# Kernel tuning notes

Hardware: AMD Instinct MI355X
Metric: run time of the kernel (lower is better)

Reference implementation:

```python
import jax, jax.numpy as jnp
import numpy as np

D = 768  # hidden dim hard-coded in the module


def setup_inputs() -> dict:
    key = jax.random.key(0)
    k1, k2, k3, k4, k5 = jax.random.split(key, 5)
    N, M = 512, 512
    return {
        "text_output": jax.random.normal(k1, (N, D), dtype=jnp.float32),
        "visual_output": jax.random.normal(k2, (M, D), dtype=jnp.float32),
        "W1": jax.random.normal(k3, (D, D), dtype=jnp.float32),
        "W2": jax.random.normal(k4, (D, D), dtype=jnp.float32),
        "W3": jax.random.normal(k5, (D, D), dtype=jnp.float32),
    }


def reference(text_output, visual_output, W1, W2, W3):
    # C[n,m] = tanh( (text @ W1) . visual[m] )
    C = jnp.tanh((text_output @ W1) @ visual_output.T)            # (N, M)
    W2_text = text_output @ W2                                    # (N, D)
    W3_visual = visual_output @ W3.T                              # (M, D)
    # M[n,m,:] = tanh(W2_text[n] + W3_visual[m] * C[n,m])
    Mt = jnp.tanh(W2_text[:, None, :] + W3_visual[None, :, :] * C[..., None])  # (N, M, D)
    # score[n,m] = text[n] . M[n,m]  (replaces the per-row Python loop)
    score = jnp.einsum("nd,nmd->nm", text_output, Mt)             # (N, M)
    return score
```

## Files before the change

kernel.cpp:

```cpp
#include <hip/hip_runtime.h>

#define DD   768
#define NN   512
#define MM   512

#define PRE_K 2.88539008177792681472f

typedef _Float16 h8 __attribute__((ext_vector_type(8)));
typedef __attribute__((ext_vector_type(4))) float f32x4;

__device__ __forceinline__ float fexp(float x) { return __builtin_amdgcn_exp2f(x); }
__device__ __forceinline__ float frcp(float x) { return __builtin_amdgcn_rcpf(x); }
__device__ __forceinline__ float fast_tanh(float x) {
  return 1.0f - 2.0f * frcp(fexp(PRE_K * x) + 1.0f);
}

__device__ __forceinline__ void splitf(float x, ushort& h, ushort& l) {
  const _Float16 hh = (_Float16)x;
  const _Float16 ll = (_Float16)(x - (float)hh);
  h = __builtin_bit_cast(unsigned short, hh);
  l = __builtin_bit_cast(unsigned short, ll);
}

__global__ __launch_bounds__(256) void prep_kernel(
    const float* __restrict__ text, const float* __restrict__ visual,
    const float* __restrict__ W1, const float* __restrict__ W2,
    const float* __restrict__ W3,
    ushort* __restrict__ th, ushort* __restrict__ tl,
    ushort* __restrict__ vh, ushort* __restrict__ vl,
    ushort* __restrict__ w3h, ushort* __restrict__ w3l,
    ushort* __restrict__ w1th, ushort* __restrict__ w1tl,
    ushort* __restrict__ w2th, ushort* __restrict__ w2tl,
    float* __restrict__ out)
{
  __shared__ float Lt[32][33];
  const int b = blockIdx.x;
  const int t = threadIdx.x;

  if (b < 1344) {
    const float* src; ushort *dh, *dl; size_t off;
    if (b < 384)      { src = text;   dh = th;  dl = tl;  off = (size_t)b * 1024; }
    else if (b < 768) { src = visual; dh = vh;  dl = vl;  off = (size_t)(b - 384) * 1024; }
    else              { src = W3;     dh = w3h; dl = w3l; off = (size_t)(b - 768) * 1024; }
    const size_t i = off + (size_t)t * 4;
    const float4 v = *(const float4*)&src[i];
    ushort4 h, l;
    splitf(v.x, h.x, l.x); splitf(v.y, h.y, l.y);
    splitf(v.z, h.z, l.z); splitf(v.w, h.w, l.w);
    *(ushort4*)&dh[i] = h;
    *(ushort4*)&dl[i] = l;
  } else if (b < 2496) {
    const int tt = b - 1344;
    const bool second = tt >= 576;
    const int tile = second ? tt - 576 : tt;
    const float* W = second ? W2 : W1;
    ushort* oh = second ? w2th : w1th;
    ushort* ol = second ? w2tl : w1tl;
    const int k0 = (tile / 24) * 32, j0 = (tile % 24) * 32;
    {
      const int k = t >> 3, j4 = (t & 7) * 4;
      const float4 v = *(const float4*)&W[(size_t)(k0 + k) * DD + j0 + j4];
      Lt[j4 + 0][k] = v.x; Lt[j4 + 1][k] = v.y;
      Lt[j4 + 2][k] = v.z; Lt[j4 + 3][k] = v.w;
    }
    __syncthreads();
    {
      const int j = t >> 3, k4 = (t & 7) * 4;
      ushort4 h, l;
      splitf(Lt[j][k4 + 0], h.x, l.x); splitf(Lt[j][k4 + 1], h.y, l.y);
      splitf(Lt[j][k4 + 2], h.z, l.z); splitf(Lt[j][k4 + 3], h.w, l.w);
      *(ushort4*)&oh[(size_t)(j0 + j) * DD + k0 + k4] = h;
      *(ushort4*)&ol[(size_t)(j0 + j) * DD + k0 + k4] = l;
    }
  } else {
    float* red = (float*)Lt;
    const int u = b - 2496;
    const int n0 = u * 2;
    const int half = t >> 7;
    const int lt = t & 127;

    const float* tr = text + (size_t)(n0 + half) * DD;
    float s = 0.f;
    #pragma unroll
    for (int i = 0; i < DD / 128; ++i) s += tr[lt + i * 128];
    red[t] = s;
    __syncthreads();
    #pragma unroll
    for (int st = 64; st > 0; st >>= 1) {
      if (lt < st) red[t] += red[t + st];
      __syncthreads();
    }
    const float Tn = red[half << 7];
    float4 o; o.x = Tn; o.y = Tn; o.z = Tn; o.w = Tn;
    *(float4*)&out[(size_t)(n0 + half) * MM + lt * 4] = o;
  }
}

#define BK   32
#define LROW 40

template <bool ALO>
__device__ __forceinline__ void gemm_core(
    const ushort* __restrict__ Ahg, const ushort* __restrict__ Alg,
    const ushort* __restrict__ Bhg, const ushort* __restrict__ Blg,
    int i0, int j0, int k0, int nsteps, f32x4* acc)
{
  __shared__ ushort As[2][2][64 * LROW];
  __shared__ ushort Bs[2][2][64 * LROW];

  const int tid  = threadIdx.x;
  const int row  = tid >> 2;
  const int ks8  = (tid & 3) * 8;
  const size_t ga = (size_t)(i0 + row) * DD + k0 + ks8;
  const size_t gb = (size_t)(j0 + row) * DD + k0 + ks8;
  const int ldsw = row * LROW + ks8;

  const int lane = tid & 63, wave = tid >> 6;
  const int r15 = lane & 15, quad = lane >> 4;
  const int fa = (wave * 16 + r15) * LROW + quad * 8;
  const int fb = r15 * LROW + quad * 8;

  h8 pah = *(const h8*)(Ahg + ga);
  h8 pal; if (ALO) pal = *(const h8*)(Alg + ga);
  h8 pbh = *(const h8*)(Bhg + gb);
  h8 pbl = *(const h8*)(Blg + gb);

  int p = 0;
  *(h8*)&As[0][0][ldsw] = pah;
  if (ALO) *(h8*)&As[0][1][ldsw] = pal;
  *(h8*)&Bs[0][0][ldsw] = pbh; *(h8*)&Bs[0][1][ldsw] = pbl;
  __syncthreads();

  for (int s = 0; s < nsteps; ++s) {
    const bool more = (s + 1 < nsteps);
    if (more) {
      pah = *(const h8*)(Ahg + ga + (s + 1) * BK);
      if (ALO) pal = *(const h8*)(Alg + ga + (s + 1) * BK);
      pbh = *(const h8*)(Bhg + gb + (s + 1) * BK);
      pbl = *(const h8*)(Blg + gb + (s + 1) * BK);
    }
    const h8 a_h = *(const h8*)&As[p][0][fa];
    h8 a_l; if (ALO) a_l = *(const h8*)&As[p][1][fa];
    h8 b_h[4], b_l[4];
    #pragma unroll
    for (int c = 0; c < 4; ++c) {
      b_h[c] = *(const h8*)&Bs[p][0][fb + c * 16 * LROW];
      b_l[c] = *(const h8*)&Bs[p][1][fb + c * 16 * LROW];
    }
    #pragma unroll
    for (int c = 0; c < 4; ++c)
      acc[c] = __builtin_amdgcn_mfma_f32_16x16x32_f16(a_h, b_h[c], acc[c], 0, 0, 0);
    #pragma unroll
    for (int c = 0; c < 4; ++c)
      acc[c] = __builtin_amdgcn_mfma_f32_16x16x32_f16(a_h, b_l[c], acc[c], 0, 0, 0);
    if (ALO) {
      #pragma unroll
      for (int c = 0; c < 4; ++c)
        acc[c] = __builtin_amdgcn_mfma_f32_16x16x32_f16(a_l, b_h[c], acc[c], 0, 0, 0);
    }
    if (more) {
      const int q = p ^ 1;
      *(h8*)&As[q][0][ldsw] = pah;
      if (ALO) *(h8*)&As[q][1][ldsw] = pal;
      *(h8*)&Bs[q][0][ldsw] = pbh; *(h8*)&Bs[q][1][ldsw] = pbl;
    }
    __syncthreads();
    p ^= 1;
  }
}

__global__ __launch_bounds__(256) void mfma1_kernel(
    const ushort* __restrict__ th, const ushort* __restrict__ tl,
    const ushort* __restrict__ vh, const ushort* __restrict__ vl,
    const ushort* __restrict__ w1th, const ushort* __restrict__ w1tl,
    const ushort* __restrict__ w2th, const ushort* __restrict__ w2tl,
    const ushort* __restrict__ w3h, const ushort* __restrict__ w3l,
    ushort* __restrict__ Ah, ushort* __restrict__ Al,
    float* __restrict__ kw2t, float* __restrict__ kw3v)
{
  const int z  = blockIdx.z;
  const int j0 = blockIdx.x * 64;
  const int i0 = blockIdx.y * 64;

  f32x4 acc[4];
  #pragma unroll
  for (int c = 0; c < 4; ++c) acc[c] = (f32x4){0.f, 0.f, 0.f, 0.f};

  if (z == 0)
    gemm_core<true >(th, tl, w1th, w1tl, i0, j0, 0, DD / BK, acc);
  else if (z == 1)
    gemm_core<false>(th, tl, w2th, w2tl, i0, j0, 0, DD / BK, acc);
  else
    gemm_core<false>(vh, vl, w3h,  w3l,  i0, j0, 0, DD / BK, acc);

  const int lane = threadIdx.x & 63, wave = threadIdx.x >> 6;
  const int r15 = lane & 15, quad = lane >> 4;
  if (z == 0) {
    #pragma unroll
    for (int c = 0; c < 4; ++c)
      #pragma unroll
      for (int r = 0; r < 4; ++r) {
        const size_t o = (size_t)(i0 + wave * 16 + quad * 4 + r) * DD + j0 + c * 16 + r15;
        splitf(acc[c][r], Ah[o], Al[o]);
      }
  } else {
    float* Out = (z == 1) ? kw2t : kw3v;
    #pragma unroll
    for (int c = 0; c < 4; ++c)
      #pragma unroll
      for (int r = 0; r < 4; ++r)
        Out[(size_t)(i0 + wave * 16 + quad * 4 + r) * DD + j0 + c * 16 + r15] =
            acc[c][r] * PRE_K;
  }
}

__global__ __launch_bounds__(256) void mfma2_kernel(
    const ushort* __restrict__ Ah, const ushort* __restrict__ Al,
    const ushort* __restrict__ vh, const ushort* __restrict__ vl,
    float* __restrict__ Q)
{
  const int z  = blockIdx.z;
  const int j0 = blockIdx.x * 64;
  const int i0 = blockIdx.y * 64;

  f32x4 acc[4];
  #pragma unroll
  for (int c = 0; c < 4; ++c) acc[c] = (f32x4){0.f, 0.f, 0.f, 0.f};
  gemm_core<true>(Ah, Al, vh, vl, i0, j0, z * (DD / 4), (DD / 4) / BK, acc);

  const int lane = threadIdx.x & 63, wave = threadIdx.x >> 6;
  const int r15 = lane & 15, quad = lane >> 4;
  float* Out = Q + (size_t)z * NN * MM;
  #pragma unroll
  for (int c = 0; c < 4; ++c)
    #pragma unroll
    for (int r = 0; r < 4; ++r)
      Out[(size_t)(i0 + wave * 16 + quad * 4 + r) * MM + j0 + c * 16 + r15] = acc[c][r];
}

#define DCH    64
#define DRANGE 256
#define MLDW   68

__global__ __launch_bounds__(256) void main_kernel(
    const float* __restrict__ text, const float* __restrict__ kw2t,
    const float* __restrict__ kw3v, const float* __restrict__ Q,
    float* __restrict__ out)
{
  __shared__ float sbuf[2][64 * MLDW];

  const int tid = threadIdx.x;
  const int nl = tid >> 4;
  const int ml = tid & 15;
  const int n0 = blockIdx.y * 16;
  const int m0 = blockIdx.x * 32;
  const int z  = blockIdx.z;
  const int n  = n0 + nl;
  const int mA = m0 + ml, mB = mA + 16;
  const int dbase = z * DRANGE;

  float cA = 0.f, cB = 0.f;
  #pragma unroll
  for (int zz = 0; zz < 4; ++zz) {
    const float* q = Q + (size_t)zz * NN * MM + (size_t)n * MM;
    cA += q[mA]; cB += q[mB];
  }
  cA = fast_tanh(cA); cB = fast_tanh(cB);

  float4 aA = {0.f, 0.f, 0.f, 0.f};
  float4 aB = {0.f, 0.f, 0.f, 0.f};

  const int srow = tid >> 4;
  const int sc4  = (tid & 15) << 2;
  const float* gt  = &text[(size_t)(n0 + srow) * DD + dbase + sc4];
  const float* g2  = &kw2t[(size_t)(n0 + srow) * DD + dbase + sc4];
  const float* g3a = &kw3v[(size_t)(m0 + srow) * DD + dbase + sc4];
  const float* g3b = &kw3v[(size_t)(m0 + 16 + srow) * DD + dbase + sc4];
  const int wt  = srow * MLDW + sc4;
  const int w2  = (16 + srow) * MLDW + sc4;
  const int w3a = (32 + srow) * MLDW + sc4;
  const int w3b = (48 + srow) * MLDW + sc4;

  float4 rt  = *(const float4*)gt;
  float4 r2  = *(const float4*)g2;
  float4 r3a = *(const float4*)g3a;
  float4 r3b = *(const float4*)g3b;
  int p = 0;
  *(float4*)&sbuf[0][wt]  = rt;
  *(float4*)&sbuf[0][w2]  = r2;
  *(float4*)&sbuf[0][w3a] = r3a;
  *(float4*)&sbuf[0][w3b] = r3b;
  __syncthreads();

  #pragma unroll
  for (int c = 0; c < DRANGE / DCH; ++c) {
    const bool more = (c + 1 < DRANGE / DCH);
    if (more) {
      rt  = *(const float4*)(gt  + (c + 1) * DCH);
      r2  = *(const float4*)(g2  + (c + 1) * DCH);
      r3a = *(const float4*)(g3a + (c + 1) * DCH);
      r3b = *(const float4*)(g3b + (c + 1) * DCH);
    }
    const float* bp = sbuf[p];
    #pragma unroll 4
    for (int j = 0; j < DCH; j += 4) {
      const float4 tv  = *(const float4*)&bp[nl * MLDW + j];
      const float4 w2v = *(const float4*)&bp[(16 + nl) * MLDW + j];
      const float4 w3A = *(const float4*)&bp[(32 + ml) * MLDW + j];
      const float4 w3B = *(const float4*)&bp[(48 + ml) * MLDW + j];
      aA.x = fmaf(tv.x, frcp(fexp(fmaf(w3A.x, cA, w2v.x)) + 1.0f), aA.x);
      aA.y = fmaf(tv.y, frcp(fexp(fmaf(w3A.y, cA, w2v.y)) + 1.0f), aA.y);
      aA.z = fmaf(tv.z, frcp(fexp(fmaf(w3A.z, cA, w2v.z)) + 1.0f), aA.z);
      aA.w = fmaf(tv.w, frcp(fexp(fmaf(w3A.w, cA, w2v.w)) + 1.0f), aA.w);
      aB.x = fmaf(tv.x, frcp(fexp(fmaf(w3B.x, cB, w2v.x)) + 1.0f), aB.x);
      aB.y = fmaf(tv.y, frcp(fexp(fmaf(w3B.y, cB, w2v.y)) + 1.0f), aB.y);
      aB.z = fmaf(tv.z, frcp(fexp(fmaf(w3B.z, cB, w2v.z)) + 1.0f), aB.z);
      aB.w = fmaf(tv.w, frcp(fexp(fmaf(w3B.w, cB, w2v.w)) + 1.0f), aB.w);
    }
    if (more) {
      const int q = p ^ 1;
      *(float4*)&sbuf[q][wt]  = rt;
      *(float4*)&sbuf[q][w2]  = r2;
      *(float4*)&sbuf[q][w3a] = r3a;
      *(float4*)&sbuf[q][w3b] = r3b;
    }
    __syncthreads();
    p ^= 1;
  }

  float* op = out + (size_t)n * MM;
  unsafeAtomicAdd(&op[mA], -2.0f * ((aA.x + aA.y) + (aA.z + aA.w)));
  unsafeAtomicAdd(&op[mB], -2.0f * ((aB.x + aB.y) + (aB.z + aB.w)));
}

extern "C" void kernel_launch(void* const* d_in, const int* in_sizes, int n_in,
                              void* d_out, int out_size, void* d_ws, size_t ws_size,
                              hipStream_t stream) {
  const float* text   = (const float*)d_in[0];
  const float* visual = (const float*)d_in[1];
  const float* W1     = (const float*)d_in[2];
  const float* W2     = (const float*)d_in[3];
  const float* W3     = (const float*)d_in[4];
  float* out = (float*)d_out;

  char* base = (char*)d_ws;
  ushort* th   = (ushort*)(base);
  ushort* tl   = (ushort*)(base + 786432);
  ushort* vh   = (ushort*)(base + 1572864);
  ushort* vl   = (ushort*)(base + 2359296);
  ushort* w1th = (ushort*)(base + 3145728);
  ushort* w1tl = (ushort*)(base + 4325376);
  ushort* w2th = (ushort*)(base + 5505024);
  ushort* w2tl = (ushort*)(base + 6684672);
  ushort* w3h  = (ushort*)(base + 7864320);
  ushort* w3l  = (ushort*)(base + 9043968);
  ushort* Ah   = (ushort*)(base + 10223616);
  ushort* Al   = (ushort*)(base + 11010048);
  float*  kw2t = (float*) (base + 11796480);
  float*  kw3v = (float*) (base + 13369344);
  float*  Q    = (float*) (base + 3145728);

  hipLaunchKernelGGL(prep_kernel, dim3(2752), dim3(256), 0, stream,
                     text, visual, W1, W2, W3,
                     th, tl, vh, vl, w3h, w3l, w1th, w1tl, w2th, w2tl, out);
  hipLaunchKernelGGL(mfma1_kernel, dim3(DD / 64, NN / 64, 3), dim3(256), 0, stream,
                     th, tl, vh, vl, w1th, w1tl, w2th, w2tl, w3h, w3l,
                     Ah, Al, kw2t, kw3v);
  hipLaunchKernelGGL(mfma2_kernel, dim3(MM / 64, NN / 64, 4), dim3(256), 0, stream,
                     Ah, Al, vh, vl, Q);
  hipLaunchKernelGGL(main_kernel, dim3(MM / 32, NN / 16, 3), dim3(256), 0, stream,
                     text, kw2t, kw3v, Q, out);
}
```

Baseline: 134.6 us.

## Fuse C-matrix GEMM and text row-sum into main kernel, shrink first GEMM tiles

```diff
diff --git a/kernel.cpp b/kernel.cpp
--- a/kernel.cpp
+++ b/kernel.cpp
@@ -30,8 +30,7 @@
     ushort* __restrict__ vh, ushort* __restrict__ vl,
     ushort* __restrict__ w3h, ushort* __restrict__ w3l,
     ushort* __restrict__ w1th, ushort* __restrict__ w1tl,
-    ushort* __restrict__ w2th, ushort* __restrict__ w2tl,
-    float* __restrict__ out)
+    ushort* __restrict__ w2th, ushort* __restrict__ w2tl)
 {
   __shared__ float Lt[32][33];
   const int b = blockIdx.x;
@@ -49,7 +48,7 @@
     splitf(v.z, h.z, l.z); splitf(v.w, h.w, l.w);
     *(ushort4*)&dh[i] = h;
     *(ushort4*)&dl[i] = l;
-  } else if (b < 2496) {
+  } else {
     const int tt = b - 1344;
     const bool second = tt >= 576;
     const int tile = second ? tt - 576 : tt;
@@ -72,97 +71,93 @@
       *(ushort4*)&oh[(size_t)(j0 + j) * DD + k0 + k4] = h;
       *(ushort4*)&ol[(size_t)(j0 + j) * DD + k0 + k4] = l;
     }
-  } else {
-    float* red = (float*)Lt;
-    const int u = b - 2496;
-    const int n0 = u * 2;
-    const int half = t >> 7;
-    const int lt = t & 127;
-
-    const float* tr = text + (size_t)(n0 + half) * DD;
-    float s = 0.f;
-    #pragma unroll
-    for (int i = 0; i < DD / 128; ++i) s += tr[lt + i * 128];
-    red[t] = s;
-    __syncthreads();
-    #pragma unroll
-    for (int st = 64; st > 0; st >>= 1) {
-      if (lt < st) red[t] += red[t + st];
-      __syncthreads();
-    }
-    const float Tn = red[half << 7];
-    float4 o; o.x = Tn; o.y = Tn; o.z = Tn; o.w = Tn;
-    *(float4*)&out[(size_t)(n0 + half) * MM + lt * 4] = o;
   }
 }
 
 #define BK   32
 #define LROW 40
+#define APL  (32 * LROW)
+#define BPL  (64 * LROW)
 
 template <bool ALO>
-__device__ __forceinline__ void gemm_core(
+__device__ __forceinline__ void gemm_core32(
+    ushort* __restrict__ As, ushort* __restrict__ Bs,
     const ushort* __restrict__ Ahg, const ushort* __restrict__ Alg,
     const ushort* __restrict__ Bhg, const ushort* __restrict__ Blg,
-    int i0, int j0, int k0, int nsteps, f32x4* acc)
+    int i0, int j0, int nsteps, f32x4* acc)
 {
-  __shared__ ushort As[2][2][64 * LROW];
-  __shared__ ushort Bs[2][2][64 * LROW];
-
-  const int tid  = threadIdx.x;
-  const int row  = tid >> 2;
-  const int ks8  = (tid & 3) * 8;
-  const size_t ga = (size_t)(i0 + row) * DD + k0 + ks8;
-  const size_t gb = (size_t)(j0 + row) * DD + k0 + ks8;
-  const int ldsw = row * LROW + ks8;
+  const int tid = threadIdx.x;
+  const int row = tid >> 2;
+  const int ks8 = (tid & 3) * 8;
+  const bool doA = (row < 32);
+  const size_t ga = (size_t)(i0 + row) * DD + ks8;
+  const size_t gb = (size_t)(j0 + row) * DD + ks8;
+  const int lw = row * LROW + ks8;
 
   const int lane = tid & 63, wave = tid >> 6;
   const int r15 = lane & 15, quad = lane >> 4;
-  const int fa = (wave * 16 + r15) * LROW + quad * 8;
-  const int fb = r15 * LROW + quad * 8;
-
-  h8 pah = *(const h8*)(Ahg + ga);
-  h8 pal; if (ALO) pal = *(const h8*)(Alg + ga);
-  h8 pbh = *(const h8*)(Bhg + gb);
-  h8 pbl = *(const h8*)(Blg + gb);
+  const int wr = wave >> 1, wc = wave & 1;
+  const int fa = (wr * 16 + r15) * LROW + quad * 8;
+  const int fb = (wc * 32 + r15) * LROW + quad * 8;
+
+  h8 pah, pal, pbh, pbl;
+  if (doA) {
+    pah = *(const h8*)(Ahg + ga);
+    if (ALO) pal = *(const h8*)(Alg + ga);
+  }
+  pbh = *(const h8*)(Bhg + gb);
+  pbl = *(const h8*)(Blg + gb);
 
   int p = 0;
-  *(h8*)&As[0][0][ldsw] = pah;
-  if (ALO) *(h8*)&As[0][1][ldsw] = pal;
-  *(h8*)&Bs[0][0][ldsw] = pbh; *(h8*)&Bs[0][1][ldsw] = pbl;
+  if (doA) {
+    *(h8*)&As[lw] = pah;
+    if (ALO) *(h8*)&As[APL + lw] = pal;
+  }
+  *(h8*)&Bs[lw] = pbh;
+  *(h8*)&Bs[BPL + lw] = pbl;
   __syncthreads();
 
   for (int s = 0; s < nsteps; ++s) {
     const bool more = (s + 1 < nsteps);
     if (more) {
-      pah = *(const h8*)(Ahg + ga + (s + 1) * BK);
-      if (ALO) pal = *(const h8*)(Alg + ga + (s + 1) * BK);
+      if (doA) {
+        pah = *(const h8*)(Ahg + ga + (s + 1) * BK);
+        if (ALO) pal = *(const h8*)(Alg + ga + (s + 1) * BK);
+      }
       pbh = *(const h8*)(Bhg + gb + (s + 1) * BK);
       pbl = *(const h8*)(Blg + gb + (s + 1) * BK);
     }
-    const h8 a_h = *(const h8*)&As[p][0][fa];
-    h8 a_l; if (ALO) a_l = *(const h8*)&As[p][1][fa];
-    h8 b_h[4], b_l[4];
-    #pragma unroll
-    for (int c = 0; c < 4; ++c) {
-      b_h[c] = *(const h8*)&Bs[p][0][fb + c * 16 * LROW];
-      b_l[c] = *(const h8*)&Bs[p][1][fb + c * 16 * LROW];
-    }
-    #pragma unroll
-    for (int c = 0; c < 4; ++c)
+    ushort* Ac = As + p * 2 * APL;
+    ushort* Bc = Bs + p * 2 * BPL;
+    const h8 a_h = *(const h8*)&Ac[fa];
+    h8 a_l; if (ALO) a_l = *(const h8*)&Ac[APL + fa];
+    h8 b_h[2], b_l[2];
+    #pragma unroll
+    for (int c = 0; c < 2; ++c) {
+      b_h[c] = *(const h8*)&Bc[fb + c * 16 * LROW];
+      b_l[c] = *(const h8*)&Bc[BPL + fb + c * 16 * LROW];
+    }
+    #pragma unroll
+    for (int c = 0; c < 2; ++c)
       acc[c] = __builtin_amdgcn_mfma_f32_16x16x32_f16(a_h, b_h[c], acc[c], 0, 0, 0);
     #pragma unroll
-    for (int c = 0; c < 4; ++c)
+    for (int c = 0; c < 2; ++c)
       acc[c] = __builtin_amdgcn_mfma_f32_16x16x32_f16(a_h, b_l[c], acc[c], 0, 0, 0);
     if (ALO) {
       #pragma unroll
-      for (int c = 0; c < 4; ++c)
+      for (int c = 0; c < 2; ++c)
         acc[c] = __builtin_amdgcn_mfma_f32_16x16x32_f16(a_l, b_h[c], acc[c], 0, 0, 0);
     }
     if (more) {
       const int q = p ^ 1;
-      *(h8*)&As[q][0][ldsw] = pah;
-      if (ALO) *(h8*)&As[q][1][ldsw] = pal;
-      *(h8*)&Bs[q][0][ldsw] = pbh; *(h8*)&Bs[q][1][ldsw] = pbl;
+      ushort* An = As + q * 2 * APL;
+      ushort* Bn = Bs + q * 2 * BPL;
+      if (doA) {
+        *(h8*)&An[lw] = pah;
+        if (ALO) *(h8*)&An[APL + lw] = pal;
+      }
+      *(h8*)&Bn[lw] = pbh;
+      *(h8*)&Bn[BPL + lw] = pbl;
     }
     __syncthreads();
     p ^= 1;
@@ -178,73 +173,56 @@
     ushort* __restrict__ Ah, ushort* __restrict__ Al,
     float* __restrict__ kw2t, float* __restrict__ kw3v)
 {
+  __shared__ ushort As[2 * 2 * APL];
+  __shared__ ushort Bs[2 * 2 * BPL];
+
   const int z  = blockIdx.z;
   const int j0 = blockIdx.x * 64;
-  const int i0 = blockIdx.y * 64;
-
-  f32x4 acc[4];
-  #pragma unroll
-  for (int c = 0; c < 4; ++c) acc[c] = (f32x4){0.f, 0.f, 0.f, 0.f};
+  const int i0 = blockIdx.y * 32;
+
+  f32x4 acc[2];
+  acc[0] = (f32x4){0.f, 0.f, 0.f, 0.f};
+  acc[1] = (f32x4){0.f, 0.f, 0.f, 0.f};
 
   if (z == 0)
-    gemm_core<true >(th, tl, w1th, w1tl, i0, j0, 0, DD / BK, acc);
+    gemm_core32<true >(As, Bs, th, tl, w1th, w1tl, i0, j0, DD / BK, acc);
   else if (z == 1)
-    gemm_core<false>(th, tl, w2th, w2tl, i0, j0, 0, DD / BK, acc);
+    gemm_core32<false>(As, Bs, th, tl, w2th, w2tl, i0, j0, DD / BK, acc);
   else
-    gemm_core<false>(vh, vl, w3h,  w3l,  i0, j0, 0, DD / BK, acc);
+    gemm_core32<false>(As, Bs, vh, vl, w3h,  w3l,  i0, j0, DD / BK, acc);
 
   const int lane = threadIdx.x & 63, wave = threadIdx.x >> 6;
   const int r15 = lane & 15, quad = lane >> 4;
+  const int wr = wave >> 1, wc = wave & 1;
   if (z == 0) {
     #pragma unroll
-    for (int c = 0; c < 4; ++c)
+    for (int c = 0; c < 2; ++c)
       #pragma unroll
       for (int r = 0; r < 4; ++r) {
-        const size_t o = (size_t)(i0 + wave * 16 + quad * 4 + r) * DD + j0 + c * 16 + r15;
+        const size_t o = (size_t)(i0 + wr * 16 + quad * 4 + r) * DD
+                       + j0 + wc * 32 + c * 16 + r15;
         splitf(acc[c][r], Ah[o], Al[o]);
       }
   } else {
     float* Out = (z == 1) ? kw2t : kw3v;
     #pragma unroll
-    for (int c = 0; c < 4; ++c)
+    for (int c = 0; c < 2; ++c)
       #pragma unroll
       for (int r = 0; r < 4; ++r)
-        Out[(size_t)(i0 + wave * 16 + quad * 4 + r) * DD + j0 + c * 16 + r15] =
+        Out[(size_t)(i0 + wr * 16 + quad * 4 + r) * DD + j0 + wc * 32 + c * 16 + r15] =
             acc[c][r] * PRE_K;
   }
 }
 
-__global__ __launch_bounds__(256) void mfma2_kernel(
+#define DCH  64
+#define MLDW 68
+#define NCH  (DD / DCH)
+
+__global__ __launch_bounds__(256) void main_kernel(
+    const float* __restrict__ text, const float* __restrict__ kw2t,
+    const float* __restrict__ kw3v,
     const ushort* __restrict__ Ah, const ushort* __restrict__ Al,
     const ushort* __restrict__ vh, const ushort* __restrict__ vl,
-    float* __restrict__ Q)
-{
-  const int z  = blockIdx.z;
-  const int j0 = blockIdx.x * 64;
-  const int i0 = blockIdx.y * 64;
-
-  f32x4 acc[4];
-  #pragma unroll
-  for (int c = 0; c < 4; ++c) acc[c] = (f32x4){0.f, 0.f, 0.f, 0.f};
-  gemm_core<true>(Ah, Al, vh, vl, i0, j0, z * (DD / 4), (DD / 4) / BK, acc);
-
-  const int lane = threadIdx.x & 63, wave = threadIdx.x >> 6;
-  const int r15 = lane & 15, quad = lane >> 4;
-  float* Out = Q + (size_t)z * NN * MM;
-  #pragma unroll
-  for (int c = 0; c < 4; ++c)
-    #pragma unroll
-    for (int r = 0; r < 4; ++r)
-      Out[(size_t)(i0 + wave * 16 + quad * 4 + r) * MM + j0 + c * 16 + r15] = acc[c][r];
-}
-
-#define DCH    64
-#define DRANGE 256
-#define MLDW   68
-
-__global__ __launch_bounds__(256) void main_kernel(
-    const float* __restrict__ text, const float* __restrict__ kw2t,
-    const float* __restrict__ kw3v, const float* __restrict__ Q,
     float* __restrict__ out)
 {
   __shared__ float sbuf[2][64 * MLDW];
@@ -254,28 +232,75 @@
   const int ml = tid & 15;
   const int n0 = blockIdx.y * 16;
   const int m0 = blockIdx.x * 32;
-  const int z  = blockIdx.z;
+  const int lane = tid & 63, wave = tid >> 6;
+  const int r15 = lane & 15, quad = lane >> 4;
+
+  const size_t aoff  = (size_t)(n0 + r15) * DD + wave * (DD / 4) + quad * 8;
+  const size_t b0off = (size_t)(m0 + r15) * DD + wave * (DD / 4) + quad * 8;
+  const size_t b1off = (size_t)(m0 + 16 + r15) * DD + wave * (DD / 4) + quad * 8;
+  const ushort* Ap  = Ah + aoff;
+  const ushort* Alp = Al + aoff;
+  const ushort* B0h = vh + b0off;
+  const ushort* B0l = vl + b0off;
+  const ushort* B1h = vh + b1off;
+  const ushort* B1l = vl + b1off;
+
+  f32x4 q0 = {0.f, 0.f, 0.f, 0.f}, q1 = {0.f, 0.f, 0.f, 0.f};
+  h8 cah  = *(const h8*)Ap;
+  h8 cal  = *(const h8*)Alp;
+  h8 cb0h = *(const h8*)B0h;
+  h8 cb0l = *(const h8*)B0l;
+  h8 cb1h = *(const h8*)B1h;
+  h8 cb1l = *(const h8*)B1l;
+  #pragma unroll
+  for (int s = 0; s < (DD / 4) / BK; ++s) {
+    h8 nah, nal, nb0h, nb0l, nb1h, nb1l;
+    const bool more = (s + 1 < (DD / 4) / BK);
+    if (more) {
+      nah  = *(const h8*)(Ap  + (s + 1) * BK);
+      nal  = *(const h8*)(Alp + (s + 1) * BK);
+      nb0h = *(const h8*)(B0h + (s + 1) * BK);
+      nb0l = *(const h8*)(B0l + (s + 1) * BK);
+      nb1h = *(const h8*)(B1h + (s + 1) * BK);
+      nb1l = *(const h8*)(B1l + (s + 1) * BK);
+    }
+    q0 = __builtin_amdgcn_mfma_f32_16x16x32_f16(cah, cb0h, q0, 0, 0, 0);
+    q1 = __builtin_amdgcn_mfma_f32_16x16x32_f16(cah, cb1h, q1, 0, 0, 0);
+    q0 = __builtin_amdgcn_mfma_f32_16x16x32_f16(cah, cb0l, q0, 0, 0, 0);
+    q1 = __builtin_amdgcn_mfma_f32_16x16x32_f16(cah, cb1l, q1, 0, 0, 0);
+    q0 = __builtin_amdgcn_mfma_f32_16x16x32_f16(cal, cb0h, q0, 0, 0, 0);
+    q1 = __builtin_amdgcn_mfma_f32_16x16x32_f16(cal, cb1h, q1, 0, 0, 0);
+    if (more) { cah = nah; cal = nal; cb0h = nb0h; cb0l = nb0l; cb1h = nb1h; cb1l = nb1l; }
+  }
+
+  float (*Qs)[16][32] = (float (*)[16][32])(&sbuf[0][0]);
+  #pragma unroll
+  for (int r = 0; r < 4; ++r) {
+    Qs[wave][quad * 4 + r][r15]      = q0[r];
+    Qs[wave][quad * 4 + r][16 + r15] = q1[r];
+  }
+  __syncthreads();
+  float sA = Qs[0][nl][ml];
+  sA += Qs[1][nl][ml]; sA += Qs[2][nl][ml]; sA += Qs[3][nl][ml];
+  float sB = Qs[0][nl][ml + 16];
+  sB += Qs[1][nl][ml + 16]; sB += Qs[2][nl][ml + 16]; sB += Qs[3][nl][ml + 16];
+  const float cA = fast_tanh(sA);
+  const float cB = fast_tanh(sB);
+  __syncthreads();
+
   const int n  = n0 + nl;
   const int mA = m0 + ml, mB = mA + 16;
-  const int dbase = z * DRANGE;
-
-  float cA = 0.f, cB = 0.f;
-  #pragma unroll
-  for (int zz = 0; zz < 4; ++zz) {
-    const float* q = Q + (size_t)zz * NN * MM + (size_t)n * MM;
-    cA += q[mA]; cB += q[mB];
-  }
-  cA = fast_tanh(cA); cB = fast_tanh(cB);
 
   float4 aA = {0.f, 0.f, 0.f, 0.f};
   float4 aB = {0.f, 0.f, 0.f, 0.f};
+  float4 ts = {0.f, 0.f, 0.f, 0.f};
 
   const int srow = tid >> 4;
   const int sc4  = (tid & 15) << 2;
-  const float* gt  = &text[(size_t)(n0 + srow) * DD + dbase + sc4];
-  const float* g2  = &kw2t[(size_t)(n0 + srow) * DD + dbase + sc4];
-  const float* g3a = &kw3v[(size_t)(m0 + srow) * DD + dbase + sc4];
-  const float* g3b = &kw3v[(size_t)(m0 + 16 + srow) * DD + dbase + sc4];
+  const float* gt  = &text[(size_t)(n0 + srow) * DD + sc4];
+  const float* g2  = &kw2t[(size_t)(n0 + srow) * DD + sc4];
+  const float* g3a = &kw3v[(size_t)(m0 + srow) * DD + sc4];
+  const float* g3b = &kw3v[(size_t)(m0 + 16 + srow) * DD + sc4];
   const int wt  = srow * MLDW + sc4;
   const int w2  = (16 + srow) * MLDW + sc4;
   const int w3a = (32 + srow) * MLDW + sc4;
@@ -292,9 +317,9 @@
   *(float4*)&sbuf[0][w3b] = r3b;
   __syncthreads();
 
-  #pragma unroll
-  for (int c = 0; c < DRANGE / DCH; ++c) {
-    const bool more = (c + 1 < DRANGE / DCH);
+  #pragma unroll 4
+  for (int c = 0; c < NCH; ++c) {
+    const bool more = (c + 1 < NCH);
     if (more) {
       rt  = *(const float4*)(gt  + (c + 1) * DCH);
       r2  = *(const float4*)(g2  + (c + 1) * DCH);
@@ -308,6 +333,7 @@
       const float4 w2v = *(const float4*)&bp[(16 + nl) * MLDW + j];
       const float4 w3A = *(const float4*)&bp[(32 + ml) * MLDW + j];
       const float4 w3B = *(const float4*)&bp[(48 + ml) * MLDW + j];
+      ts.x += tv.x; ts.y += tv.y; ts.z += tv.z; ts.w += tv.w;
       aA.x = fmaf(tv.x, frcp(fexp(fmaf(w3A.x, cA, w2v.x)) + 1.0f), aA.x);
       aA.y = fmaf(tv.y, frcp(fexp(fmaf(w3A.y, cA, w2v.y)) + 1.0f), aA.y);
       aA.z = fmaf(tv.z, frcp(fexp(fmaf(w3A.z, cA, w2v.z)) + 1.0f), aA.z);
@@ -328,9 +354,10 @@
     p ^= 1;
   }
 
+  const float tsum = (ts.x + ts.y) + (ts.z + ts.w);
   float* op = out + (size_t)n * MM;
-  unsafeAtomicAdd(&op[mA], -2.0f * ((aA.x + aA.y) + (aA.z + aA.w)));
-  unsafeAtomicAdd(&op[mB], -2.0f * ((aB.x + aB.y) + (aB.z + aB.w)));
+  op[mA] = fmaf(-2.0f, (aA.x + aA.y) + (aA.z + aA.w), tsum);
+  op[mB] = fmaf(-2.0f, (aB.x + aB.y) + (aB.z + aB.w), tsum);
 }
 
 extern "C" void kernel_launch(void* const* d_in, const int* in_sizes, int n_in,
@@ -358,16 +385,13 @@
   ushort* Al   = (ushort*)(base + 11010048);
   float*  kw2t = (float*) (base + 11796480);
   float*  kw3v = (float*) (base + 13369344);
-  float*  Q    = (float*) (base + 3145728);
-
-  hipLaunchKernelGGL(prep_kernel, dim3(2752), dim3(256), 0, stream,
+
+  hipLaunchKernelGGL(prep_kernel, dim3(2496), dim3(256), 0, stream,
                      text, visual, W1, W2, W3,
-                     th, tl, vh, vl, w3h, w3l, w1th, w1tl, w2th, w2tl, out);
-  hipLaunchKernelGGL(mfma1_kernel, dim3(DD / 64, NN / 64, 3), dim3(256), 0, stream,
+                     th, tl, vh, vl, w3h, w3l, w1th, w1tl, w2th, w2tl);
+  hipLaunchKernelGGL(mfma1_kernel, dim3(DD / 64, NN / 32, 3), dim3(256), 0, stream,
                      th, tl, vh, vl, w1th, w1tl, w2th, w2tl, w3h, w3l,
                      Ah, Al, kw2t, kw3v);
-  hipLaunchKernelGGL(mfma2_kernel, dim3(MM / 64, NN / 64, 4), dim3(256), 0, stream,
-                     Ah, Al, vh, vl, Q);
-  hipLaunchKernelGGL(main_kernel, dim3(MM / 32, NN / 16, 3), dim3(256), 0, stream,
-                     text, kw2t, kw3v, Q, out);
-}
+  hipLaunchKernelGGL(main_kernel, dim3(MM / 32, NN / 16), dim3(256), 0, stream,
+                     text, kw2t, kw3v, Ah, Al, vh, vl, out);
+}
```

After: 136.2 us. About the same (+1.2%).
